# Kernel tuning notes

Hardware: AMD Instinct MI355X
Metric: run time of the kernel (lower is better)

## Reference

```python
import jax, jax.numpy as jnp
import numpy as np

# dims
B, TQ, NQ, DQ = 2, 32, 196, 896      # batch, chunks, queries/chunk, slow-feat dim
T, H, W, CIN = 32, 8, 8, 4           # fast feature video dims
EMB = 1024                           # fast input mapping (kv) dim
HID = 512                            # cross_attn_hidden_dim
NH = 4                               # heads
HD = HID // NH                       # head dim = 128
HALF = HD // 2                       # 64 rotary freq channels
SEC = [22, 21, 21]                   # 3D rope sections (t,h,w) over the 64 freqs
FF = 2 * HID
OUT = 896
BASE = 10000.0
QGRID = 14                           # 196 = 14x14 query spatial grid
EPS = 1e-5


def _p(key, shape, scale=0.02):
    return (jax.random.normal(key, shape, dtype=jnp.float32) * scale)


def setup_inputs() -> dict:
    key = jax.random.key(0)
    ks = jax.random.split(key, 20)
    inp = {
        "x": jax.random.normal(ks[0], (B, T, H, W, CIN), dtype=jnp.float32),
        "slow_feats": jax.random.normal(ks[1], (B, TQ, NQ, DQ), dtype=jnp.float32),
        "frame_num": jnp.full((B,), T, dtype=jnp.int32),
        # query_input_mapping: 896 -> 512
        "Wq_in": _p(ks[2], (DQ, HID)), "bq_in": jnp.zeros((HID,), jnp.float32),
        # fast input_mapping (linear): 4 -> 1024
        "Wm": _p(ks[3], (CIN, EMB)), "bm": jnp.zeros((EMB,), jnp.float32),
        # cross-attn projections
        "Wq": _p(ks[4], (HID, HID)), "bq": jnp.zeros((HID,), jnp.float32),
        "Wk": _p(ks[5], (EMB, HID)), "bk": jnp.zeros((HID,), jnp.float32),
        "Wv": _p(ks[6], (EMB, HID)), "bv": jnp.zeros((HID,), jnp.float32),
        "Wo": _p(ks[7], (HID, HID)), "bo": jnp.zeros((HID,), jnp.float32),
        # decoder layer norms + FFN (dim_feedforward = 2*hidden)
        "g1": jnp.ones((HID,), jnp.float32), "be1": jnp.zeros((HID,), jnp.float32),
        "W1": _p(ks[8], (HID, FF)), "b1": jnp.zeros((FF,), jnp.float32),
        "W2": _p(ks[9], (FF, HID)), "b2": jnp.zeros((HID,), jnp.float32),
        "g2": jnp.ones((HID,), jnp.float32), "be2": jnp.zeros((HID,), jnp.float32),
        # output MLP (mlp_depth=2): 512 -> 1024 -> GELU -> 896
        "M1": _p(ks[10], (HID, 2 * HID)), "bm1": jnp.zeros((2 * HID,), jnp.float32),
        "M2": _p(ks[11], (2 * HID, OUT)), "bm2": jnp.zeros((OUT,), jnp.float32),
    }
    return inp


def _ln(x, g, b):
    m = x.mean(-1, keepdims=True)
    v = jnp.var(x, axis=-1, keepdims=True)
    return (x - m) * jax.lax.rsqrt(v + EPS) * g + b


def _rope_cos_sin(pos):
    # pos: (N,3) float (t,h,w). Qwen2-style inv_freq over head_dim=128.
    inv_freq = 1.0 / (BASE ** (jnp.arange(0, HD, 2, dtype=jnp.float32) / HD))  # (64,)
    sel = jnp.asarray([0] * SEC[0] + [1] * SEC[1] + [2] * SEC[2])              # (64,)
    freqs = pos[:, sel] * inv_freq                                             # (N,64)
    emb = jnp.concatenate([freqs, freqs], axis=-1)                             # (N,128)
    return jnp.cos(emb), jnp.sin(emb)


def _rot_half(x):
    return jnp.concatenate([-x[..., HALF:], x[..., :HALF]], axis=-1)


def _positions():
    # query tokens: (chunk t, 14x14 grid)
    qt = jnp.repeat(jnp.arange(TQ), NQ)
    qg = jnp.tile(jnp.arange(NQ), TQ)
    q_pos = jnp.stack([qt, qg // QGRID, qg % QGRID], axis=-1).astype(jnp.float32)  # (6272,3)
    # kv tokens: (frame t, HxW grid)
    kt = jnp.repeat(jnp.arange(T), H * W)
    kg = jnp.tile(jnp.arange(H * W), T)
    k_pos = jnp.stack([kt, kg // W, kg % W], axis=-1).astype(jnp.float32)          # (2048,3)
    return q_pos, k_pos


def _forward(x, slow_feats, Wq_in, bq_in, Wm, bm, Wq, bq, Wk, bk, Wv, bv,
             Wo, bo, g1, be1, W1, b1, W2, b2, g2, be2, M1, bm1, M2, bm2):
    q_pos, k_pos = _positions()
    cos_q, sin_q = _rope_cos_sin(q_pos)   # (Nq,128)
    cos_k, sin_k = _rope_cos_sin(k_pos)   # (Nk,128)
    scale = 1.0 / jnp.sqrt(jnp.float32(HD))

    def per_sample(xi, si):
        # slow feats -> queries: (32,196,896) -> (6272,512)
        q_in = (si.reshape(TQ * NQ, DQ) @ Wq_in + bq_in)
        # fast feats -> kv tokens: (T,H,W,Cin) -> (2048,1024)
        kv = (xi.reshape(T * H * W, CIN) @ Wm + bm)
        # projections -> heads
        q = (q_in @ Wq + bq).reshape(-1, NH, HD)
        k = (kv @ Wk + bk).reshape(-1, NH, HD)
        v = (kv @ Wv + bv).reshape(-1, NH, HD)
        # 3D RoPE on q and k
        q = q * cos_q[:, None, :] + _rot_half(q) * sin_q[:, None, :]
        k = k * cos_k[:, None, :] + _rot_half(k) * sin_k[:, None, :]
        # cross attention
        attn = jnp.einsum('qhd,khd->hqk', q, k) * scale
        attn = jax.nn.softmax(attn, axis=-1)
        o = jnp.einsum('hqk,khd->qhd', attn, v).reshape(-1, HID)
        o = o @ Wo + bo
        # residual + norm + FFN + norm (post-norm decoder layer)
        h = _ln(q_in + o, g1, be1)
        ff = jax.nn.gelu(h @ W1 + b1) @ W2 + b2
        h = _ln(h + ff, g2, be2)
        # output MLP: Linear -> GELU -> Linear
        y = jax.nn.gelu(h @ M1 + bm1) @ M2 + bm2
        return y  # (6272, 896)

    return jax.vmap(per_sample)(x, slow_feats)  # (B, 6272, 896)


def reference(x, slow_feats, frame_num, Wq_in, bq_in, Wm, bm, Wq, bq, Wk, bk,
              Wv, bv, Wo, bo, g1, be1, W1, b1, W2, b2, g2, be2, M1, bm1, M2, bm2):
    # frame_num is the valid-frame count per sample; here all samples are full
    # length (frame_num == T), so no KV masking is needed.
    del frame_num
    return _forward(x, slow_feats, Wq_in, bq_in, Wm, bm, Wq, bq, Wk, bk, Wv, bv,
                    Wo, bo, g1, be1, W1, b1, W2, b2, g2, be2, M1, bm1, M2, bm2)
```

## Files before the change

kernel.cpp:

```cpp
#include <hip/hip_runtime.h>
#include <cstdint>
#include <cstddef>

#define BATCH 2
#define MQ 12544
#define ROWS_Q 6272
#define MK 4096
#define ROWS_K 2048
#define HID 512
#define NH 4
#define HD 128
#define EMB 1024
#define DQ 896
#define FF 1024
#define OUTD 896

typedef __bf16 bf16;
typedef unsigned int u32;
typedef bf16 bf16x8 __attribute__((ext_vector_type(8)));
typedef bf16 bf16x4 __attribute__((ext_vector_type(4)));
typedef float f32x4 __attribute__((ext_vector_type(4)));

enum { OP_BIAS = 0, OP_GELU = 1, OP_RES = 2 };

__device__ __forceinline__ float gelu_tanh(float x) {
    float x3 = x * x * x;
    return 0.5f * x * (1.0f + tanhf(0.7978845608028654f * (x + 0.044715f * x3)));
}

__device__ __forceinline__ void gld16(const bf16* g, bf16* l) {
    __builtin_amdgcn_global_load_lds(
        (const __attribute__((address_space(1))) unsigned int*)g,
        (__attribute__((address_space(3))) unsigned int*)l, 16, 0, 0);
}

__device__ __forceinline__ u32 pack_bf16(float a, float b) {
    union { bf16 h[2]; u32 w; } u;
    u.h[0] = (bf16)a; u.h[1] = (bf16)b;
    return u.w;
}

template <int OP, bool WF32, bool WB16>
__global__ __launch_bounds__(256) void mgemm(
    const bf16* __restrict__ A, const bf16* __restrict__ Bt,
    const float* __restrict__ bias, const float* __restrict__ res,
    float* __restrict__ Cf, bf16* __restrict__ Cb, int M, int N, int K)
{
    __shared__ __align__(16) bf16 As[128 * 32];
    __shared__ __align__(16) bf16 Bs[128 * 32];
    const int tid  = threadIdx.x;
    const int m0   = blockIdx.y * 128;
    const int n0   = blockIdx.x * 128;
    const int wave = tid >> 6, lane = tid & 63;
    const int wm = (wave >> 1) * 64, wn = (wave & 1) * 64;

    f32x4 acc[4][4] = {};

    const int srow = tid >> 2;
    const int scol = (tid & 3) * 8;
    const bf16* Ag = A  + (size_t)(m0 + srow) * K + scol;
    const bf16* Bg = Bt + (size_t)(n0 + srow) * K + scol;
    bf16* Al = &As[tid * 8];
    bf16* Bl = &Bs[tid * 8];
    const size_t half = (size_t)64 * K;

    const int fr = lane & 15;
    const int kq = (lane >> 4) * 8;
    const bf16* pa = &As[(wm + fr) * 32 + kq];
    const bf16* pb = &Bs[(wn + fr) * 32 + kq];

    for (int k0 = 0; k0 < K; k0 += 32) {
        gld16(Ag + k0,        Al);
        gld16(Ag + k0 + half, Al + 64 * 32);
        gld16(Bg + k0,        Bl);
        gld16(Bg + k0 + half, Bl + 64 * 32);
        __syncthreads();

        bf16x8 af[4], bfr[4];
        #pragma unroll
        for (int i = 0; i < 4; ++i) af[i]  = *(const bf16x8*)(pa + i * 16 * 32);
        #pragma unroll
        for (int j = 0; j < 4; ++j) bfr[j] = *(const bf16x8*)(pb + j * 16 * 32);
        #pragma unroll
        for (int i = 0; i < 4; ++i)
            #pragma unroll
            for (int j = 0; j < 4; ++j)
                acc[i][j] = __builtin_amdgcn_mfma_f32_16x16x32_bf16(
                    af[i], bfr[j], acc[i][j], 0, 0, 0);
        __syncthreads();
    }

    const int colb = n0 + wn + (lane & 15);
    const int rowb = m0 + wm + (lane >> 4) * 4;
    #pragma unroll
    for (int i = 0; i < 4; ++i) {
        #pragma unroll
        for (int j = 0; j < 4; ++j) {
            const int c = colb + j * 16;
            const float bj = bias[c];
            #pragma unroll
            for (int r = 0; r < 4; ++r) {
                const int m = rowb + i * 16 + r;
                float v = acc[i][j][r] + bj;
                if (OP == OP_GELU) v = gelu_tanh(v);
                if (OP == OP_RES)  v += res[(size_t)m * N + c];
                if (WF32) Cf[(size_t)m * N + c] = v;
                if (WB16) Cb[(size_t)m * N + c] = (bf16)v;
            }
        }
    }
}

template <int OP, bool WF32, bool WB16>
__global__ __launch_bounds__(256) void mgemm64(
    const bf16* __restrict__ A, const bf16* __restrict__ Bt,
    const float* __restrict__ bias, const float* __restrict__ res,
    float* __restrict__ Cf, bf16* __restrict__ Cb, int M, int N, int K)
{
    __shared__ __align__(16) bf16 As[64 * 32];
    __shared__ __align__(16) bf16 Bs[128 * 32];
    const int tid  = threadIdx.x;
    const int m0   = blockIdx.y * 64;
    const int n0   = blockIdx.x * 128;
    const int wave = tid >> 6, lane = tid & 63;
    const int wm = (wave >> 1) * 32, wn = (wave & 1) * 64;

    f32x4 acc[2][4] = {};

    const int srow = tid >> 2;
    const int scol = (tid & 3) * 8;
    const bf16* Ag = A  + (size_t)(m0 + srow) * K + scol;
    const bf16* Bg = Bt + (size_t)(n0 + srow) * K + scol;
    bf16* Al = &As[tid * 8];
    bf16* Bl = &Bs[tid * 8];
    const size_t half = (size_t)64 * K;

    const int fr = lane & 15;
    const int kq = (lane >> 4) * 8;
    const bf16* pa = &As[(wm + fr) * 32 + kq];
    const bf16* pb = &Bs[(wn + fr) * 32 + kq];

    for (int k0 = 0; k0 < K; k0 += 32) {
        gld16(Ag + k0,        Al);
        gld16(Bg + k0,        Bl);
        gld16(Bg + k0 + half, Bl + 64 * 32);
        __syncthreads();

        bf16x8 af[2], bfr[4];
        #pragma unroll
        for (int i = 0; i < 2; ++i) af[i]  = *(const bf16x8*)(pa + i * 16 * 32);
        #pragma unroll
        for (int j = 0; j < 4; ++j) bfr[j] = *(const bf16x8*)(pb + j * 16 * 32);
        #pragma unroll
        for (int i = 0; i < 2; ++i)
            #pragma unroll
            for (int j = 0; j < 4; ++j)
                acc[i][j] = __builtin_amdgcn_mfma_f32_16x16x32_bf16(
                    af[i], bfr[j], acc[i][j], 0, 0, 0);
        __syncthreads();
    }

    const int colb = n0 + wn + (lane & 15);
    const int rowb = m0 + wm + (lane >> 4) * 4;
    #pragma unroll
    for (int i = 0; i < 2; ++i) {
        #pragma unroll
        for (int j = 0; j < 4; ++j) {
            const int c = colb + j * 16;
            const float bj = bias[c];
            #pragma unroll
            for (int r = 0; r < 4; ++r) {
                const int m = rowb + i * 16 + r;
                float v = acc[i][j][r] + bj;
                if (OP == OP_GELU) v = gelu_tanh(v);
                if (OP == OP_RES)  v += res[(size_t)m * N + c];
                if (WF32) Cf[(size_t)m * N + c] = v;
                if (WB16) Cb[(size_t)m * N + c] = (bf16)v;
            }
        }
    }
}

struct TDesc { const float* src; bf16* dst; int K; int N; int tile0; };
struct TDescs { TDesc d[9]; };

__global__ __launch_bounds__(256) void transpose_all(TDescs td)
{
    __shared__ float t[32][33];
    const int blk = blockIdx.x;
    int i = 0;
    #pragma unroll
    for (int j = 1; j < 9; ++j) if (blk >= td.d[j].tile0) i = j;
    const float* src = td.d[i].src;
    bf16* dst = td.d[i].dst;
    const int K = td.d[i].K, N = td.d[i].N;
    const int local = blk - td.d[i].tile0;
    const int ntx = N >> 5;
    const int bx = local % ntx, by = local / ntx;
    const int x = threadIdx.x & 31, y = threadIdx.x >> 5;
    #pragma unroll
    for (int p = 0; p < 32; p += 8)
        t[y + p][x] = src[(size_t)(by * 32 + y + p) * N + bx * 32 + x];
    __syncthreads();
    #pragma unroll
    for (int p = 0; p < 32; p += 8)
        dst[(size_t)(bx * 32 + y + p) * K + by * 32 + x] = (bf16)t[x][y + p];
}

__global__ __launch_bounds__(256) void cvt_kernel(
    const float* __restrict__ in, bf16* __restrict__ out, int n4)
{
    int i = blockIdx.x * 256 + threadIdx.x;
    if (i >= n4) return;
    float4 v = ((const float4*)in)[i];
    out[4 * i + 0] = (bf16)v.x;
    out[4 * i + 1] = (bf16)v.y;
    out[4 * i + 2] = (bf16)v.z;
    out[4 * i + 3] = (bf16)v.w;
}

__global__ __launch_bounds__(256) void kv_kernel(
    const float* __restrict__ x, const float* __restrict__ Wm,
    const float* __restrict__ bm, bf16* __restrict__ kv)
{
    int idx = blockIdx.x * 256 + threadIdx.x;
    int r = idx >> 10, n = idx & 1023;
    float4 xv = *(const float4*)(x + (size_t)r * 4);
    float v = bm[n] + xv.x * Wm[n] + xv.y * Wm[1024 + n]
                    + xv.z * Wm[2048 + n] + xv.w * Wm[3072 + n];
    kv[idx] = (bf16)v;
}

__global__ __launch_bounds__(256) void rope_b_kernel(
    const bf16* __restrict__ in, bf16* __restrict__ out,
    int tok, int gdiv, int wdiv, int total, float sc, int istr, int icoff)
{
    int idx = blockIdx.x * 256 + threadIdx.x;
    if (idx >= total) return;
    int row = idx >> 7;
    int r2 = idx & 127;
    int h = r2 >> 5;
    int j2 = r2 & 31;
    int j = 2 * j2;
    int n = row % tok;
    int t = n / gdiv;
    int g = n % gdiv;
    int gh = g / wdiv;
    int gw = g % wdiv;
    float pa = (j < 22) ? (float)t : (j < 43) ? (float)gh : (float)gw;
    int j1 = j + 1;
    float pb = (j1 < 22) ? (float)t : (j1 < 43) ? (float)gh : (float)gw;
    float fra = pa * exp2f(-(float)j  * 0.20762050593045954f);
    float frb = pb * exp2f(-(float)j1 * 0.20762050593045954f);
    float ca = cosf(fra), sa = sinf(fra);
    float cb = cosf(frb), sb = sinf(frb);
    size_t ibase = (size_t)row * istr + icoff + (size_t)h * 128 + j;
    size_t obase = (size_t)row * 512 + (size_t)h * 128 + j;
    union { u32 w; bf16 e[2]; } ua, ub;
    ua.w = *(const u32*)(in + ibase);
    ub.w = *(const u32*)(in + ibase + 64);
    float x1a = (float)ua.e[0], x1b = (float)ua.e[1];
    float x2a = (float)ub.e[0], x2b = (float)ub.e[1];
    *(u32*)(out + obase)      = pack_bf16((x1a * ca - x2a * sa) * sc,
                                          (x1b * cb - x2b * sb) * sc);
    *(u32*)(out + obase + 64) = pack_bf16((x2a * ca + x1a * sa) * sc,
                                          (x2b * cb + x1b * sb) * sc);
}

__global__ __launch_bounds__(256) void vt_tiled(
    const bf16* __restrict__ kv16, bf16* __restrict__ vt)
{
    __shared__ bf16 t[64][72];
    const int tt = blockIdx.x * 64;
    const int d0 = blockIdx.y * 64;
    const int bh = blockIdx.z;
    const int b = bh >> 2, h = bh & 3;
    const int rr = threadIdx.x >> 4;
    const int cc = (threadIdx.x & 15) * 4;
    #pragma unroll
    for (int p = 0; p < 4; ++p) {
        int r = rr + p * 16;
        *(bf16x4*)&t[r][cc] = *(const bf16x4*)
            (kv16 + (size_t)(b * ROWS_K + tt + r) * 1024 + 512 + h * 128 + d0 + cc);
    }
    __syncthreads();
    #pragma unroll
    for (int p = 0; p < 4; ++p) {
        int r = rr + p * 16;
        bf16x4 v;
        v[0] = t[cc + 0][r]; v[1] = t[cc + 1][r];
        v[2] = t[cc + 2][r]; v[3] = t[cc + 3][r];
        *(bf16x4*)(vt + (size_t)bh * HD * ROWS_K + (size_t)(d0 + r) * ROWS_K + tt + cc) = v;
    }
}

__global__ __launch_bounds__(256) void ln_kernel(
    float* __restrict__ xb, const float* __restrict__ g,
    const float* __restrict__ be, bf16* __restrict__ out16)
{
    int wave = threadIdx.x >> 6, lane = threadIdx.x & 63;
    size_t row = (size_t)blockIdx.x * 4 + wave;
    float* xp = xb + row * 512;
    float4 a = ((const float4*)xp)[lane];
    float4 b = ((const float4*)xp)[lane + 64];
    float s  = a.x + a.y + a.z + a.w + b.x + b.y + b.z + b.w;
    float sq = a.x*a.x + a.y*a.y + a.z*a.z + a.w*a.w
             + b.x*b.x + b.y*b.y + b.z*b.z + b.w*b.w;
    #pragma unroll
    for (int off = 32; off; off >>= 1) {
        s  += __shfl_xor(s, off);
        sq += __shfl_xor(sq, off);
    }
    float mean = s * (1.0f / 512.0f);
    float var  = sq * (1.0f / 512.0f) - mean * mean;
    float rstd = rsqrtf(var + 1e-5f);
    float4 gv1 = ((const float4*)g)[lane],  gv2 = ((const float4*)g)[lane + 64];
    float4 bv1 = ((const float4*)be)[lane], bv2 = ((const float4*)be)[lane + 64];
    a.x = (a.x - mean) * rstd * gv1.x + bv1.x;
    a.y = (a.y - mean) * rstd * gv1.y + bv1.y;
    a.z = (a.z - mean) * rstd * gv1.z + bv1.z;
    a.w = (a.w - mean) * rstd * gv1.w + bv1.w;
    b.x = (b.x - mean) * rstd * gv2.x + bv2.x;
    b.y = (b.y - mean) * rstd * gv2.y + bv2.y;
    b.z = (b.z - mean) * rstd * gv2.z + bv2.z;
    b.w = (b.w - mean) * rstd * gv2.w + bv2.w;
    ((float4*)xp)[lane]      = a;
    ((float4*)xp)[lane + 64] = b;
    bf16* op = out16 + row * 512;
    *(u32*)(op + lane * 4)       = pack_bf16(a.x, a.y);
    *(u32*)(op + lane * 4 + 2)   = pack_bf16(a.z, a.w);
    *(u32*)(op + 256 + lane * 4)     = pack_bf16(b.x, b.y);
    *(u32*)(op + 256 + lane * 4 + 2) = pack_bf16(b.z, b.w);
}

__global__ __launch_bounds__(256, 2) void mattn_kernel(
    const bf16* __restrict__ qs, const bf16* __restrict__ ks,
    const bf16* __restrict__ vt, bf16* __restrict__ outb)
{
    __shared__ __align__(16) char smem[35840];
    bf16* Ksh = (bf16*)smem;
    bf16* Vsh = (bf16*)(smem + 17408);

    const int tid = threadIdx.x;
    const int wave = tid >> 6, lane = tid & 63;
    const int quad = lane >> 4, c = lane & 15;
    const int bid = blockIdx.x;
    const int qt = bid % 49;
    const int h  = (bid / 49) & 3;
    const int b  = bid / 196;

    const int q0 = qt * 128 + wave * 32;
    const bf16* qg = qs + (size_t)(b * ROWS_Q + q0) * HID + h * HD;
    const bf16* kg = ks + (size_t)(b * ROWS_K) * HID + h * HD;
    const bf16* vg = vt + (size_t)(b * NH + h) * HD * ROWS_K;

    bf16x8 qf[2][4];
    #pragma unroll
    for (int n = 0; n < 2; ++n)
        #pragma unroll
        for (int s = 0; s < 4; ++s)
            qf[n][s] = *(const bf16x8*)(qg + (size_t)(n * 16 + c) * HID + s * 32 + quad * 8);

    f32x4 o[8][2] = {};
    float m_i[2] = {-1e30f, -1e30f}, l_i[2] = {0.0f, 0.0f};

    const int st_t = tid >> 2;
    const int st_d = (tid & 3) * 32;
    const int sv_d = tid >> 1;
    const int sv_t = (tid & 1) * 32;

    for (int kt = 0; kt < 32; ++kt) {
        __syncthreads();
        {
            const bf16* src = kg + (size_t)(kt * 64 + st_t) * HID + st_d;
            bf16* dst = Ksh + st_t * 136 + st_d;
            #pragma unroll
            for (int i = 0; i < 4; ++i)
                *(bf16x8*)(dst + i * 8) = *(const bf16x8*)(src + i * 8);
        }
        {
            const bf16* src = vg + (size_t)sv_d * ROWS_K + kt * 64 + sv_t;
            bf16* dst = Vsh + sv_d * 72 + sv_t;
            #pragma unroll
            for (int i = 0; i < 4; ++i)
                *(bf16x8*)(dst + i * 8) = *(const bf16x8*)(src + i * 8);
        }
        __syncthreads();

        f32x4 s[4][2] = {};
        #pragma unroll
        for (int ksi = 0; ksi < 4; ++ksi) {
            bf16x8 kf[4];
            #pragma unroll
            for (int mi = 0; mi < 4; ++mi)
                kf[mi] = *(const bf16x8*)(Ksh + (mi * 16 + c) * 136 + ksi * 32 + quad * 8);
            #pragma unroll
            for (int mi = 0; mi < 4; ++mi)
                #pragma unroll
                for (int n = 0; n < 2; ++n)
                    s[mi][n] = __builtin_amdgcn_mfma_f32_16x16x32_bf16(
                        kf[mi], qf[n][ksi], s[mi][n], 0, 0, 0);
        }

        float alpha[2];
        #pragma unroll
        for (int n = 0; n < 2; ++n) {
            float mx = -1e30f;
            #pragma unroll
            for (int mi = 0; mi < 4; ++mi)
                #pragma unroll
                for (int r = 0; r < 4; ++r) mx = fmaxf(mx, s[mi][n][r]);
            mx = fmaxf(mx, __shfl_xor(mx, 16));
            mx = fmaxf(mx, __shfl_xor(mx, 32));
            float mn = fmaxf(m_i[n], mx);
            alpha[n] = __expf(m_i[n] - mn);
            m_i[n] = mn;
            float sm = 0.0f;
            #pragma unroll
            for (int mi = 0; mi < 4; ++mi)
                #pragma unroll
                for (int r = 0; r < 4; ++r) {
                    float p = __expf(s[mi][n][r] - mn);
                    s[mi][n][r] = p;
                    sm += p;
                }
            sm += __shfl_xor(sm, 16);
            sm += __shfl_xor(sm, 32);
            l_i[n] = l_i[n] * alpha[n] + sm;
            #pragma unroll
            for (int md = 0; md < 8; ++md) {
                o[md][n][0] *= alpha[n]; o[md][n][1] *= alpha[n];
                o[md][n][2] *= alpha[n]; o[md][n][3] *= alpha[n];
            }
        }

        u32 pk[4][2][2];
        #pragma unroll
        for (int mi = 0; mi < 4; ++mi)
            #pragma unroll
            for (int n = 0; n < 2; ++n) {
                pk[mi][n][0] = pack_bf16(s[mi][n][0], s[mi][n][1]);
                pk[mi][n][1] = pack_bf16(s[mi][n][2], s[mi][n][3]);
            }
        bf16x8 pf[2][2];
        #pragma unroll
        for (int kst = 0; kst < 2; ++kst)
            #pragma unroll
            for (int n = 0; n < 2; ++n) {
                union { bf16x8 v8; u32 d[4]; } u;
                #pragma unroll
                for (int dw = 0; dw < 4; ++dw) {
                    int srcl = ((quad & 1) * 2 + (dw >> 1)) * 16 + c;
                    u32 lo = (u32)__shfl((int)pk[2 * kst][n][dw & 1], srcl);
                    u32 hi = (u32)__shfl((int)pk[2 * kst + 1][n][dw & 1], srcl);
                    u.d[dw] = (quad >= 2) ? hi : lo;
                }
                pf[kst][n] = u.v8;
            }

        #pragma unroll
        for (int kst = 0; kst < 2; ++kst)
            #pragma unroll
            for (int md = 0; md < 8; ++md) {
                bf16x8 vf = *(const bf16x8*)(Vsh + (md * 16 + c) * 72 + kst * 32 + quad * 8);
                #pragma unroll
                for (int n = 0; n < 2; ++n)
                    o[md][n] = __builtin_amdgcn_mfma_f32_16x16x32_bf16(
                        vf, pf[kst][n], o[md][n], 0, 0, 0);
            }
    }

    __syncthreads();
    bf16* Osh = (bf16*)smem + wave * (32 * 136);
    float inv[2] = {1.0f / l_i[0], 1.0f / l_i[1]};
    #pragma unroll
    for (int md = 0; md < 8; ++md)
        #pragma unroll
        for (int n = 0; n < 2; ++n)
            #pragma unroll
            for (int hh = 0; hh < 2; ++hh) {
                u32 w = pack_bf16(o[md][n][2 * hh] * inv[n], o[md][n][2 * hh + 1] * inv[n]);
                int d = md * 16 + quad * 4 + 2 * hh;
                int qq = n * 16 + c;
                *(u32*)(Osh + qq * 136 + d) = w;
            }
    __syncthreads();
    bf16* og = outb + (size_t)(b * ROWS_Q + q0) * HID + h * HD;
    #pragma unroll
    for (int i = 0; i < 8; ++i) {
        int idx = i * 64 + lane;
        int qq = idx >> 4;
        int ch = idx & 15;
        bf16x8 vv = *(const bf16x8*)(Osh + qq * 136 + ch * 8);
        *(bf16x8*)(og + (size_t)qq * HID + ch * 8) = vv;
    }
}

extern "C" void kernel_launch(void* const* d_in, const int* in_sizes, int n_in,
                              void* d_out, int out_size, void* d_ws, size_t ws_size,
                              hipStream_t stream)
{
    const float* x     = (const float*)d_in[0];
    const float* slow  = (const float*)d_in[1];
    const float* Wq_in = (const float*)d_in[3];
    const float* bq_in = (const float*)d_in[4];
    const float* Wm    = (const float*)d_in[5];
    const float* bm    = (const float*)d_in[6];
    const float* Wq    = (const float*)d_in[7];
    const float* bq    = (const float*)d_in[8];
    const float* Wk    = (const float*)d_in[9];
    const float* bk    = (const float*)d_in[10];
    const float* Wv    = (const float*)d_in[11];
    const float* bv    = (const float*)d_in[12];
    const float* Wo    = (const float*)d_in[13];
    const float* bo    = (const float*)d_in[14];
    const float* g1    = (const float*)d_in[15];
    const float* be1   = (const float*)d_in[16];
    const float* W1    = (const float*)d_in[17];
    const float* b1    = (const float*)d_in[18];
    const float* W2    = (const float*)d_in[19];
    const float* b2    = (const float*)d_in[20];
    const float* g2    = (const float*)d_in[21];
    const float* be2   = (const float*)d_in[22];
    const float* M1    = (const float*)d_in[23];
    const float* bm1   = (const float*)d_in[24];
    const float* M2    = (const float*)d_in[25];
    const float* bm2   = (const float*)d_in[26];
    float* out = (float*)d_out;

    float* q_in_f = (float*)d_ws;
    float* ob     = q_in_f + (size_t)MQ * HID;
    float* bkv    = ob + (size_t)MQ * HID;
    bf16* shared_b = (bf16*)(bkv + 1024);
    bf16* q_in_b = shared_b + (size_t)MQ * FF;
    bf16* kv_b   = q_in_b + (size_t)MQ * HID;
    bf16* h_b    = kv_b + (size_t)MK * EMB;
    bf16* q16    = h_b + (size_t)MQ * HID;
    bf16* kv16   = q16 + (size_t)MQ * HID;
    bf16* qbt    = kv16 + (size_t)MK * EMB;
    bf16* kbt    = qbt + (size_t)MQ * HID;
    bf16* Vt     = kbt + (size_t)MK * HID;
    bf16* Wq_in_t = Vt + (size_t)8 * HD * ROWS_K;
    bf16* Wq_t  = Wq_in_t + 512 * 896;
    bf16* kvw_t = Wq_t + 512 * 512;
    bf16* Wo_t  = kvw_t + 1024 * 1024;
    bf16* W1_t  = Wo_t + 512 * 512;
    bf16* W2_t  = W1_t + 1024 * 512;
    bf16* M1_t  = W2_t + 512 * 1024;
    bf16* M2_t  = M1_t + 1024 * 512;
    bf16* slow_b = shared_b;
    bf16* attn_b = shared_b;
    bf16* ff1_b  = shared_b;
    bf16* m1_b   = shared_b;

    dim3 blk(256);

    TDescs td;
    int t0 = 0;
    auto set = [&](int i, const float* s, bf16* d, int K, int N) {
        td.d[i] = {s, d, K, N, t0};
        t0 += (N / 32) * (K / 32);
    };
    set(0, Wq_in, Wq_in_t, 896, 512);
    set(1, Wq,    Wq_t,    512, 512);
    set(2, Wk,    kvw_t,              1024, 512);
    set(3, Wv,    kvw_t + 512 * 1024, 1024, 512);
    set(4, Wo,    Wo_t,    512, 512);
    set(5, W1,    W1_t,    512, 1024);
    set(6, W2,    W2_t,    1024, 512);
    set(7, M1,    M1_t,    512, 1024);
    set(8, M2,    M2_t,    1024, 896);
    transpose_all<<<t0, blk, 0, stream>>>(td);

    hipMemcpyAsync(bkv,       bk, 512 * sizeof(float), hipMemcpyDeviceToDevice, stream);
    hipMemcpyAsync(bkv + 512, bv, 512 * sizeof(float), hipMemcpyDeviceToDevice, stream);

    cvt_kernel<<<(MQ * DQ / 4 + 255) / 256, blk, 0, stream>>>(slow, slow_b, MQ * DQ / 4);
    kv_kernel<<<(MK * EMB) / 256, blk, 0, stream>>>(x, Wm, bm, kv_b);

    mgemm64<OP_BIAS, true, true><<<dim3(4, 196), blk, 0, stream>>>(
        slow_b, Wq_in_t, bq_in, nullptr, q_in_f, q_in_b, MQ, HID, DQ);
    mgemm64<OP_BIAS, false, true><<<dim3(4, 196), blk, 0, stream>>>(
        q_in_b, Wq_t, bq, nullptr, nullptr, q16, MQ, HID, HID);
    mgemm64<OP_BIAS, false, true><<<dim3(8, 64), blk, 0, stream>>>(
        kv_b, kvw_t, bkv, nullptr, nullptr, kv16, MK, 1024, EMB);
    rope_b_kernel<<<(MQ * 128 + 255) / 256, blk, 0, stream>>>(
        q16, qbt, ROWS_Q, 196, 14, MQ * 128, 0.08838834764831843f, 512, 0);
    rope_b_kernel<<<(MK * 128 + 255) / 256, blk, 0, stream>>>(
        kv16, kbt, ROWS_K, 64, 8, MK * 128, 1.0f, 1024, 0);
    vt_tiled<<<dim3(32, 2, 8), blk, 0, stream>>>(kv16, Vt);
    mattn_kernel<<<dim3(392), blk, 0, stream>>>(qbt, kbt, Vt, attn_b);
    mgemm64<OP_RES, true, false><<<dim3(4, 196), blk, 0, stream>>>(
        attn_b, Wo_t, bo, q_in_f, ob, nullptr, MQ, HID, HID);
    ln_kernel<<<MQ / 4, blk, 0, stream>>>(ob, g1, be1, h_b);
    mgemm<OP_GELU, false, true><<<dim3(8, 98), blk, 0, stream>>>(
        h_b, W1_t, b1, nullptr, nullptr, ff1_b, MQ, FF, HID);
    mgemm64<OP_RES, true, false><<<dim3(4, 196), blk, 0, stream>>>(
        ff1_b, W2_t, b2, ob, q_in_f, nullptr, MQ, HID, FF);
    ln_kernel<<<MQ / 4, blk, 0, stream>>>(q_in_f, g2, be2, h_b);
    mgemm<OP_GELU, false, true><<<dim3(8, 98), blk, 0, stream>>>(
        h_b, M1_t, bm1, nullptr, nullptr, m1_b, MQ, 2 * HID, HID);
    mgemm<OP_BIAS, true, false><<<dim3(7, 98), blk, 0, stream>>>(
        m1_b, M2_t, bm2, nullptr, out, nullptr, MQ, OUTD, 2 * HID);
}
```

Measured before the change: 582.3 us.

## Process K=64 per barrier in GEMMs and interleave attention block order by batch-head

Both GEMM kernels now load two 32-wide K slices into separate LDS buffers per iteration and run MFMAs on both before syncing. This halves the number of barriers and keeps more global loads in flight, at the cost of twice the LDS per block, which may lower occupancy. The attention kernel's block index mapping now puts batch/head in the low bits, so consecutive blocks cover different heads of the same query tile. This changes which K/V data blocks running at the same time share in cache.

```diff
diff --git a/kernel.cpp b/kernel.cpp
--- a/kernel.cpp
+++ b/kernel.cpp
@@ -46,8 +46,10 @@
     const float* __restrict__ bias, const float* __restrict__ res,
     float* __restrict__ Cf, bf16* __restrict__ Cb, int M, int N, int K)
 {
-    __shared__ __align__(16) bf16 As[128 * 32];
-    __shared__ __align__(16) bf16 Bs[128 * 32];
+    __shared__ __align__(16) bf16 As0[128 * 32];
+    __shared__ __align__(16) bf16 As1[128 * 32];
+    __shared__ __align__(16) bf16 Bs0[128 * 32];
+    __shared__ __align__(16) bf16 Bs1[128 * 32];
     const int tid  = threadIdx.x;
     const int m0   = blockIdx.y * 128;
     const int n0   = blockIdx.x * 128;
@@ -60,33 +62,56 @@
     const int scol = (tid & 3) * 8;
     const bf16* Ag = A  + (size_t)(m0 + srow) * K + scol;
     const bf16* Bg = Bt + (size_t)(n0 + srow) * K + scol;
-    bf16* Al = &As[tid * 8];
-    bf16* Bl = &Bs[tid * 8];
+    bf16* Al0 = &As0[tid * 8];
+    bf16* Al1 = &As1[tid * 8];
+    bf16* Bl0 = &Bs0[tid * 8];
+    bf16* Bl1 = &Bs1[tid * 8];
     const size_t half = (size_t)64 * K;
 
     const int fr = lane & 15;
     const int kq = (lane >> 4) * 8;
-    const bf16* pa = &As[(wm + fr) * 32 + kq];
-    const bf16* pb = &Bs[(wn + fr) * 32 + kq];
-
-    for (int k0 = 0; k0 < K; k0 += 32) {
-        gld16(Ag + k0,        Al);
-        gld16(Ag + k0 + half, Al + 64 * 32);
-        gld16(Bg + k0,        Bl);
-        gld16(Bg + k0 + half, Bl + 64 * 32);
+    const bf16* pa0 = &As0[(wm + fr) * 32 + kq];
+    const bf16* pa1 = &As1[(wm + fr) * 32 + kq];
+    const bf16* pb0 = &Bs0[(wn + fr) * 32 + kq];
+    const bf16* pb1 = &Bs1[(wn + fr) * 32 + kq];
+
+    for (int k0 = 0; k0 < K; k0 += 64) {
+        gld16(Ag + k0,             Al0);
+        gld16(Ag + k0 + half,      Al0 + 64 * 32);
+        gld16(Bg + k0,             Bl0);
+        gld16(Bg + k0 + half,      Bl0 + 64 * 32);
+        gld16(Ag + k0 + 32,        Al1);
+        gld16(Ag + k0 + 32 + half, Al1 + 64 * 32);
+        gld16(Bg + k0 + 32,        Bl1);
+        gld16(Bg + k0 + 32 + half, Bl1 + 64 * 32);
         __syncthreads();
 
-        bf16x8 af[4], bfr[4];
-        #pragma unroll
-        for (int i = 0; i < 4; ++i) af[i]  = *(const bf16x8*)(pa + i * 16 * 32);
-        #pragma unroll
-        for (int j = 0; j < 4; ++j) bfr[j] = *(const bf16x8*)(pb + j * 16 * 32);
-        #pragma unroll
-        for (int i = 0; i < 4; ++i)
-            #pragma unroll
-            for (int j = 0; j < 4; ++j)
-                acc[i][j] = __builtin_amdgcn_mfma_f32_16x16x32_bf16(
-                    af[i], bfr[j], acc[i][j], 0, 0, 0);
+        {
+            bf16x8 af[4], bfr[4];
+            #pragma unroll
+            for (int i = 0; i < 4; ++i) af[i]  = *(const bf16x8*)(pa0 + i * 16 * 32);
+            #pragma unroll
+            for (int j = 0; j < 4; ++j) bfr[j] = *(const bf16x8*)(pb0 + j * 16 * 32);
+            #pragma unroll
+            for (int i = 0; i < 4; ++i)
+                #pragma unroll
+                for (int j = 0; j < 4; ++j)
+                    acc[i][j] = __builtin_amdgcn_mfma_f32_16x16x32_bf16(
+                        af[i], bfr[j], acc[i][j], 0, 0, 0);
+        }
+        {
+            bf16x8 af[4], bfr[4];
+            #pragma unroll
+            for (int i = 0; i < 4; ++i) af[i]  = *(const bf16x8*)(pa1 + i * 16 * 32);
+            #pragma unroll
+            for (int j = 0; j < 4; ++j) bfr[j] = *(const bf16x8*)(pb1 + j * 16 * 32);
+            #pragma unroll
+            for (int i = 0; i < 4; ++i)
+                #pragma unroll
+                for (int j = 0; j < 4; ++j)
+                    acc[i][j] = __builtin_amdgcn_mfma_f32_16x16x32_bf16(
+                        af[i], bfr[j], acc[i][j], 0, 0, 0);
+        }
         __syncthreads();
     }
 
@@ -117,8 +142,10 @@
     const float* __restrict__ bias, const float* __restrict__ res,
     float* __restrict__ Cf, bf16* __restrict__ Cb, int M, int N, int K)
 {
-    __shared__ __align__(16) bf16 As[64 * 32];
-    __shared__ __align__(16) bf16 Bs[128 * 32];
+    __shared__ __align__(16) bf16 As0[64 * 32];
+    __shared__ __align__(16) bf16 As1[64 * 32];
+    __shared__ __align__(16) bf16 Bs0[128 * 32];
+    __shared__ __align__(16) bf16 Bs1[128 * 32];
     const int tid  = threadIdx.x;
     const int m0   = blockIdx.y * 64;
     const int n0   = blockIdx.x * 128;
@@ -131,32 +158,54 @@
     const int scol = (tid & 3) * 8;
     const bf16* Ag = A  + (size_t)(m0 + srow) * K + scol;
     const bf16* Bg = Bt + (size_t)(n0 + srow) * K + scol;
-    bf16* Al = &As[tid * 8];
-    bf16* Bl = &Bs[tid * 8];
+    bf16* Al0 = &As0[tid * 8];
+    bf16* Al1 = &As1[tid * 8];
+    bf16* Bl0 = &Bs0[tid * 8];
+    bf16* Bl1 = &Bs1[tid * 8];
     const size_t half = (size_t)64 * K;
 
     const int fr = lane & 15;
     const int kq = (lane >> 4) * 8;
-    const bf16* pa = &As[(wm + fr) * 32 + kq];
-    const bf16* pb = &Bs[(wn + fr) * 32 + kq];
-
-    for (int k0 = 0; k0 < K; k0 += 32) {
-        gld16(Ag + k0,        Al);
-        gld16(Bg + k0,        Bl);
-        gld16(Bg + k0 + half, Bl + 64 * 32);
+    const bf16* pa0 = &As0[(wm + fr) * 32 + kq];
+    const bf16* pa1 = &As1[(wm + fr) * 32 + kq];
+    const bf16* pb0 = &Bs0[(wn + fr) * 32 + kq];
+    const bf16* pb1 = &Bs1[(wn + fr) * 32 + kq];
+
+    for (int k0 = 0; k0 < K; k0 += 64) {
+        gld16(Ag + k0,             Al0);
+        gld16(Bg + k0,             Bl0);
+        gld16(Bg + k0 + half,      Bl0 + 64 * 32);
+        gld16(Ag + k0 + 32,        Al1);
+        gld16(Bg + k0 + 32,        Bl1);
+        gld16(Bg + k0 + 32 + half, Bl1 + 64 * 32);
         __syncthreads();
 
-        bf16x8 af[2], bfr[4];
-        #pragma unroll
-        for (int i = 0; i < 2; ++i) af[i]  = *(const bf16x8*)(pa + i * 16 * 32);
-        #pragma unroll
-        for (int j = 0; j < 4; ++j) bfr[j] = *(const bf16x8*)(pb + j * 16 * 32);
-        #pragma unroll
-        for (int i = 0; i < 2; ++i)
-            #pragma unroll
-            for (int j = 0; j < 4; ++j)
-                acc[i][j] = __builtin_amdgcn_mfma_f32_16x16x32_bf16(
-                    af[i], bfr[j], acc[i][j], 0, 0, 0);
+        {
+            bf16x8 af[2], bfr[4];
+            #pragma unroll
+            for (int i = 0; i < 2; ++i) af[i]  = *(const bf16x8*)(pa0 + i * 16 * 32);
+            #pragma unroll
+            for (int j = 0; j < 4; ++j) bfr[j] = *(const bf16x8*)(pb0 + j * 16 * 32);
+            #pragma unroll
+            for (int i = 0; i < 2; ++i)
+                #pragma unroll
+                for (int j = 0; j < 4; ++j)
+                    acc[i][j] = __builtin_amdgcn_mfma_f32_16x16x32_bf16(
+                        af[i], bfr[j], acc[i][j], 0, 0, 0);
+        }
+        {
+            bf16x8 af[2], bfr[4];
+            #pragma unroll
+            for (int i = 0; i < 2; ++i) af[i]  = *(const bf16x8*)(pa1 + i * 16 * 32);
+            #pragma unroll
+            for (int j = 0; j < 4; ++j) bfr[j] = *(const bf16x8*)(pb1 + j * 16 * 32);
+            #pragma unroll
+            for (int i = 0; i < 2; ++i)
+                #pragma unroll
+                for (int j = 0; j < 4; ++j)
+                    acc[i][j] = __builtin_amdgcn_mfma_f32_16x16x32_bf16(
+                        af[i], bfr[j], acc[i][j], 0, 0, 0);
+        }
         __syncthreads();
     }
 
@@ -345,9 +394,10 @@
     const int wave = tid >> 6, lane = tid & 63;
     const int quad = lane >> 4, c = lane & 15;
     const int bid = blockIdx.x;
-    const int qt = bid % 49;
-    const int h  = (bid / 49) & 3;
-    const int b  = bid / 196;
+    const int bh = bid & 7;
+    const int qt = bid >> 3;
+    const int h  = bh & 3;
+    const int b  = bh >> 2;
 
     const int q0 = qt * 128 + wave * 32;
     const bf16* qg = qs + (size_t)(b * ROWS_Q + q0) * HID + h * HD;
```

Result: faster. 569.9 us (-2.1%).
